# Performance work log

Hardware: AMD Instinct MI355X
Metric: run time of the kernel (lower is better)

The kernel has to match this reference:

```python
import jax, jax.numpy as jnp
import numpy as np

N_NODES = 100000
N_EDGES = 3200000
IN_DIM = 128
H_GCN = 64
H_LSTM = 64


def setup_inputs() -> dict:
    key = jax.random.key(0)
    ks = jax.random.split(key, 12)
    s = 0.05
    return {
        "x": jax.random.normal(ks[0], (IN_DIM, N_NODES), dtype=jnp.float32),
        "edge_index": jax.random.randint(ks[1], (2, N_EDGES), 0, N_NODES, dtype=jnp.int32),
        "W1": jax.random.normal(ks[2], (IN_DIM, H_GCN), dtype=jnp.float32) * s,
        "b1": jnp.zeros((H_GCN,), dtype=jnp.float32),
        "W2": jax.random.normal(ks[3], (H_GCN, H_GCN), dtype=jnp.float32) * s,
        "b2": jnp.zeros((H_GCN,), dtype=jnp.float32),
        "w_ih": jax.random.normal(ks[4], (4 * H_LSTM, H_GCN), dtype=jnp.float32) * s,
        "w_hh": jax.random.normal(ks[5], (4 * H_LSTM, H_LSTM), dtype=jnp.float32) * s,
        "b_ih": jax.random.normal(ks[6], (4 * H_LSTM,), dtype=jnp.float32) * s,
        "b_hh": jax.random.normal(ks[7], (4 * H_LSTM,), dtype=jnp.float32) * s,
        "fc_w": jax.random.normal(ks[8], (1, H_LSTM), dtype=jnp.float32) * s,
        "fc_b": jnp.zeros((1,), dtype=jnp.float32),
    }


def gcn_conv(x, src, dst, n, W, b):
    # PyG GCNConv: add self loops, symmetric norm D^-1/2 (A+I) D^-1/2, linear-first.
    h = x @ W  # [N, out]
    loop = jnp.arange(n, dtype=src.dtype)
    s = jnp.concatenate([src, loop])
    d = jnp.concatenate([dst, loop])
    deg = jax.ops.segment_sum(jnp.ones(d.shape, dtype=h.dtype), d, num_segments=n)
    dinv = jnp.where(deg > 0, jax.lax.rsqrt(deg), 0.0)
    norm = dinv[s] * dinv[d]  # [E+N]
    out = jax.ops.segment_sum(h[s] * norm[:, None], d, num_segments=n)
    return out + b


def reference(x, edge_index, W1, b1, W2, b2, w_ih, w_hh, b_ih, b_hh, fc_w, fc_b):
    xt = x.T  # data.x.T -> [N, input_dim]
    n = xt.shape[0]
    src, dst = edge_index[0], edge_index[1]
    h = jax.nn.relu(gcn_conv(xt, src, dst, n, W1, b1))
    h = gcn_conv(h, src, dst, n, W2, b2)
    z = h[0][None, :]  # [1, H_GCN] node 0 embedding
    # single-step LSTM, zero initial state (h0=c0=0)
    gates = z @ w_ih.T + b_ih + b_hh  # [1, 4H]
    i, f, g, o = jnp.split(gates, 4, axis=-1)
    c = jax.nn.sigmoid(i) * jnp.tanh(g)  # f*c0 = 0
    hy = jax.nn.sigmoid(o) * jnp.tanh(c)  # [1, H_LSTM]
    y = hy @ fc_w.T + fc_b  # [1, 1]
    return y[:, :, None]  # [1, 1, 1]
```

## Files before the change

### kernel.cpp

```cpp
#include <hip/hip_runtime.h>
#include <math.h>

#define N_NODES 100000
#define N_EDGES 3200000
#define IN_DIM 128
#define HG 64

#define E0CAP 2048
#define MCAP  65536
#define NBMW  3125
#define SCAN_BLOCKS 1024
#define BLK_E0 16

#define OFF_DEG       0u
#define OFF_SLOTMAP   400000u
#define OFF_CNT       800000u
#define OFF_ACC       800032u
#define OFF_BMS1      1324320u
#define OFF_BMNEED    1336864u
#define WS_ZERO_BYTES 1349408u
#define OFF_BCNT      1349408u
#define OFF_BLIST     1353504u
#define OFF_EDGES0    1419040u
#define OFF_SLOTNODE  1427232u
#define OFF_MLISTS    1435424u
#define OFF_MLISTD    1697568u

__device__ __forceinline__ float dinv_of(int degv) {
    return 1.0f / sqrtf((float)(degv + 1));
}

__global__ void k_scan0(const int* __restrict__ src, const int* __restrict__ dst,
                        int4* __restrict__ zbase, int* __restrict__ bcnt,
                        int* __restrict__ blist) {
    __shared__ int lcnt;
    __shared__ int lsrc[BLK_E0];
    if (threadIdx.x == 0) lcnt = 0;
    __syncthreads();
    int tid = blockIdx.x * blockDim.x + threadIdx.x;
    int nth = gridDim.x * blockDim.x;
    const int nz = WS_ZERO_BYTES / 16;
    int4 z; z.x = 0; z.y = 0; z.z = 0; z.w = 0;
    for (int i = tid; i < nz; i += nth) zbase[i] = z;
    const int4* dst4 = (const int4*)dst;
    const int n4 = N_EDGES / 4;
    for (int i = tid; i < n4; i += nth) {
        int4 dv = dst4[i];
        int ds[4] = {dv.x, dv.y, dv.z, dv.w};
#pragma unroll
        for (int k = 0; k < 4; k++) {
            if (ds[k] == 0) {
                int p = atomicAdd(&lcnt, 1);
                if (p < BLK_E0) lsrc[p] = src[4 * i + k];
            }
        }
    }
    __syncthreads();
    int c = lcnt; if (c > BLK_E0) c = BLK_E0;
    if (threadIdx.x == 0) bcnt[blockIdx.x] = c;
    for (int i = threadIdx.x; i < c; i += blockDim.x)
        blist[blockIdx.x * BLK_E0 + i] = lsrc[i];
}

__global__ void k_build_slots(const int* __restrict__ bcnt, const int* __restrict__ blist,
                              int* __restrict__ edges0, int* __restrict__ slotnodes,
                              int* __restrict__ slotmap, int* __restrict__ cnt,
                              unsigned* __restrict__ bmS1) {
    const int t = threadIdx.x;
    for (int b = t; b < SCAN_BLOCKS; b += blockDim.x) {
        int c = bcnt[b];
        if (c > 0) {
            int p = atomicAdd(&cnt[0], c);
            for (int j = 0; j < c && p + j < E0CAP; j++)
                edges0[p + j] = blist[b * BLK_E0 + j];
        }
    }
    __syncthreads();
    int n0 = atomicAdd(&cnt[0], 0); if (n0 > E0CAP) n0 = E0CAP;
    for (int i = t; i < n0 + 1; i += blockDim.x) {
        int s = (i == n0) ? 0 : edges0[i];
        if (atomicCAS(&slotmap[s], 0, 1) == 0) {
            int p = atomicAdd(&cnt[1], 1);
            if (p < E0CAP) slotnodes[p] = s;
        }
    }
    __syncthreads();
    int ns = atomicAdd(&cnt[1], 0); if (ns > E0CAP) ns = E0CAP;
    for (int i = t; i < ns; i += blockDim.x) {
        int s = slotnodes[i];
        slotmap[s] = i + 1;
        atomicOr(&bmS1[s >> 5], 1u << (s & 31));
    }
}

__global__ void k_match(const int* __restrict__ src, const int* __restrict__ dst,
                        const int* __restrict__ slotmap,
                        const unsigned* __restrict__ bmS1, unsigned* __restrict__ bmNeed,
                        int* __restrict__ cnt, int* __restrict__ mlistS,
                        int* __restrict__ mlistD) {
    __shared__ unsigned sbm[NBMW];
    for (int i = threadIdx.x; i < NBMW; i += blockDim.x) sbm[i] = bmS1[i];
    __syncthreads();
    int tid = blockIdx.x * blockDim.x + threadIdx.x;
    int nth = gridDim.x * blockDim.x;
    const int4* dst4 = (const int4*)dst;
    const int n4 = N_EDGES / 4;
    for (int i = tid; i < n4; i += nth) {
        int4 dv = dst4[i];
        unsigned ds[4] = {(unsigned)dv.x, (unsigned)dv.y, (unsigned)dv.z, (unsigned)dv.w};
#pragma unroll
        for (int k = 0; k < 4; k++) {
            unsigned d = ds[k];
            if ((sbm[d >> 5] >> (d & 31)) & 1u) {
                int e = 4 * i + k;
                int s = src[e];
                int sl = slotmap[d] - 1;
                int p = atomicAdd(&cnt[2], 1);
                if (p < MCAP) {
                    mlistS[p] = s | (sl << 17);
                    mlistD[p] = (int)d;
                }
                atomicOr(&bmNeed[s >> 5], 1u << (s & 31));
            }
        }
    }
}

__global__ void k_deg_need(const int* __restrict__ dst, const unsigned* __restrict__ bmS1,
                           const unsigned* __restrict__ bmNeed, int* __restrict__ deg) {
    __shared__ unsigned sbm[NBMW];
    for (int i = threadIdx.x; i < NBMW; i += blockDim.x) sbm[i] = bmS1[i] | bmNeed[i];
    __syncthreads();
    int tid = blockIdx.x * blockDim.x + threadIdx.x;
    int nth = gridDim.x * blockDim.x;
    const int4* dst4 = (const int4*)dst;
    const int n4 = N_EDGES / 4;
    for (int i = tid; i < n4; i += nth) {
        int4 dv = dst4[i];
        unsigned ds[4] = {(unsigned)dv.x, (unsigned)dv.y, (unsigned)dv.z, (unsigned)dv.w};
#pragma unroll
        for (int k = 0; k < 4; k++) {
            unsigned d = ds[k];
            if ((sbm[d >> 5] >> (d & 31)) & 1u) atomicAdd(&deg[d], 1);
        }
    }
}

__global__ void k_contrib(const int* __restrict__ deg, const int* __restrict__ cnt,
                          const int* __restrict__ mlistS, const int* __restrict__ mlistD,
                          const int* __restrict__ slotnodes,
                          const float* __restrict__ x, const float* __restrict__ W1,
                          float* __restrict__ acc) {
    int m = cnt[2]; if (m > MCAP) m = MCAP;
    int ns = cnt[1]; if (ns > E0CAP) ns = E0CAP;
    const int vtotal = 2 * (m + ns);
    const int j = threadIdx.x;
    for (int v = blockIdx.x; v < vtotal; v += gridDim.x) {
        const int ii = v >> 1;
        const int kbase = (v & 1) << 6;
        int s, sl;
        float w;
        if (ii < m) {
            int sw = mlistS[ii];
            int d = mlistD[ii];
            s = sw & 0x1FFFF;
            sl = sw >> 17;
            w = dinv_of(deg[s]) * dinv_of(deg[d]);
        } else {
            sl = ii - m;
            s = slotnodes[sl];
            float dv = dinv_of(deg[s]);
            w = dv * dv;
        }
        const float* xp = x + (size_t)kbase * N_NODES + s;
        const float* wp = W1 + kbase * HG + j;
        float g = 0.f;
#pragma unroll
        for (int k = 0; k < 64; k++) {
            g = fmaf(xp[(size_t)k * N_NODES], wp[k * HG], g);
        }
        atomicAdd(&acc[sl * HG + j], g * w);
    }
}

#define CHUNK 256
__global__ void k_final(const float* __restrict__ b1, const float* __restrict__ W2,
                        const float* __restrict__ b2, const float* __restrict__ w_ih,
                        const float* __restrict__ b_ih, const float* __restrict__ b_hh,
                        const float* __restrict__ fc_w, const float* __restrict__ fc_b,
                        const int* __restrict__ deg, const int* __restrict__ slotmap,
                        const int* __restrict__ cnt, const int* __restrict__ edges0,
                        const float* __restrict__ acc, float* __restrict__ out) {
    __shared__ int   sh_sl[CHUNK];
    __shared__ float sh_w[CHUNK];
    __shared__ float partial[4][HG];
    __shared__ float agg[HG];
    __shared__ float zv[HG];
    __shared__ float gates[4 * HG];
    __shared__ float hw[HG];
    const int t = threadIdx.x;
    const int ch = t & (HG - 1);
    const int grp = t >> 6;
    int n0 = cnt[0]; if (n0 > E0CAP) n0 = E0CAP;

    const float dinv0 = dinv_of(deg[0]);
    const float bch = b1[ch];

    float a = 0.f;
    for (int base = 0; base < n0; base += CHUNK) {
        int cn = n0 - base; if (cn > CHUNK) cn = CHUNK;
        __syncthreads();
        if (t < cn) {
            int s = edges0[base + t];
            sh_sl[t] = slotmap[s] - 1;
            sh_w[t] = dinv_of(deg[s]) * dinv0;
        }
        __syncthreads();
        for (int i = grp; i < cn; i += 4) {
            float h = acc[sh_sl[i] * HG + ch] + bch;
            a = fmaf(sh_w[i], (h > 0.f ? h : 0.f), a);
        }
    }
    partial[grp][ch] = a;
    __syncthreads();
    if (t < HG) {
        int sl0 = slotmap[0] - 1;
        float h0 = acc[sl0 * HG + t] + b1[t];
        float s = dinv0 * dinv0 * (h0 > 0.f ? h0 : 0.f);
        s += partial[0][t] + partial[1][t] + partial[2][t] + partial[3][t];
        agg[t] = s;
    }
    __syncthreads();

    if (t < HG) {
        float zz = b2[t];
#pragma unroll 8
        for (int k = 0; k < HG; k++) zz = fmaf(agg[k], W2[k * HG + t], zz);
        zv[t] = zz;
    }
    __syncthreads();

    {
        float gt = b_ih[t] + b_hh[t];
#pragma unroll 8
        for (int jj = 0; jj < HG; jj++) gt = fmaf(zv[jj], w_ih[t * HG + jj], gt);
        gates[t] = gt;
    }
    __syncthreads();

    if (t < HG) {
        float ig = 1.f / (1.f + expf(-gates[t]));
        float gg = tanhf(gates[2 * HG + t]);
        float og = 1.f / (1.f + expf(-gates[3 * HG + t]));
        float c = ig * gg;
        float hy = og * tanhf(c);
        hw[t] = hy * fc_w[t];
    }
    __syncthreads();
    if (t == 0) {
        float y = fc_b[0];
        for (int jj = 0; jj < HG; jj++) y += hw[jj];
        out[0] = y;
    }
}

extern "C" void kernel_launch(void* const* d_in, const int* in_sizes, int n_in,
                              void* d_out, int out_size, void* d_ws, size_t ws_size,
                              hipStream_t stream) {
    const float* x    = (const float*)d_in[0];
    const int*   ei   = (const int*)d_in[1];
    const float* W1   = (const float*)d_in[2];
    const float* b1   = (const float*)d_in[3];
    const float* W2   = (const float*)d_in[4];
    const float* b2   = (const float*)d_in[5];
    const float* w_ih = (const float*)d_in[6];
    const float* b_ih = (const float*)d_in[8];
    const float* b_hh = (const float*)d_in[9];
    const float* fc_w = (const float*)d_in[10];
    const float* fc_b = (const float*)d_in[11];
    float* out = (float*)d_out;

    const int* src = ei;
    const int* dst = ei + N_EDGES;

    char* ws = (char*)d_ws;
    int*      deg       = (int*)(ws + OFF_DEG);
    int*      slotmap   = (int*)(ws + OFF_SLOTMAP);
    int*      cnt       = (int*)(ws + OFF_CNT);
    float*    acc       = (float*)(ws + OFF_ACC);
    unsigned* bmS1      = (unsigned*)(ws + OFF_BMS1);
    unsigned* bmNeed    = (unsigned*)(ws + OFF_BMNEED);
    int*      bcnt      = (int*)(ws + OFF_BCNT);
    int*      blist     = (int*)(ws + OFF_BLIST);
    int*      edges0    = (int*)(ws + OFF_EDGES0);
    int*      slotnodes = (int*)(ws + OFF_SLOTNODE);
    int*      mlistS    = (int*)(ws + OFF_MLISTS);
    int*      mlistD    = (int*)(ws + OFF_MLISTD);

    k_scan0<<<SCAN_BLOCKS, 256, 0, stream>>>(src, dst, (int4*)ws, bcnt, blist);
    k_build_slots<<<1, 256, 0, stream>>>(bcnt, blist, edges0, slotnodes, slotmap, cnt, bmS1);
    k_match<<<SCAN_BLOCKS, 256, 0, stream>>>(src, dst, slotmap, bmS1, bmNeed, cnt,
                                             mlistS, mlistD);
    k_deg_need<<<SCAN_BLOCKS, 256, 0, stream>>>(dst, bmS1, bmNeed, deg);
    k_contrib<<<4096, 64, 0, stream>>>(deg, cnt, mlistS, mlistD, slotnodes, x, W1, acc);
    k_final<<<1, 256, 0, stream>>>(b1, W2, b2, w_ih, b_ih, b_hh, fc_w, fc_b,
                                   deg, slotmap, cnt, edges0, acc, out);
}
```

Baseline: 168.8 us.

## Fuse six-kernel pipeline into one cooperative kernel with grid syncs

Merges the scan, slot-building, match, degree, contribution and final LSTM kernels into a single cooperative launch of 768 blocks that separates phases with grid.sync(). The aim is to remove the launch overhead and inter-kernel gaps of six small launches. Workspace values written by other blocks are now read with atomic reads to keep them coherent across the grid. The cost is grid-wide barriers, fewer blocks for the streaming edge scans, and a contribution phase re-partitioned into four 64-thread workers per block.

```diff
diff --git a/kernel.cpp b/kernel.cpp
--- a/kernel.cpp
+++ b/kernel.cpp
@@ -1,5 +1,8 @@
 #include <hip/hip_runtime.h>
+#include <hip/hip_cooperative_groups.h>
 #include <math.h>
+
+namespace cg = cooperative_groups;
 
 #define N_NODES 100000
 #define N_EDGES 3200000
@@ -9,8 +12,9 @@
 #define E0CAP 2048
 #define MCAP  65536
 #define NBMW  3125
-#define SCAN_BLOCKS 1024
+#define FUSED_BLOCKS 768
 #define BLK_E0 16
+#define CHUNK 256
 
 #define OFF_DEG       0u
 #define OFF_SLOTMAP   400000u
@@ -26,85 +30,98 @@
 #define OFF_MLISTS    1435424u
 #define OFF_MLISTD    1697568u
 
+struct KParams {
+    const int *src, *dst;
+    const float *x, *W1, *b1, *W2, *b2, *w_ih, *b_ih, *b_hh, *fc_w, *fc_b;
+    int *deg, *slotmap, *cnt;
+    float *acc;
+    unsigned *bmS1, *bmNeed;
+    int *bcnt, *blist, *edges0, *slotnodes, *mlistS, *mlistD;
+    float *out;
+};
+
 __device__ __forceinline__ float dinv_of(int degv) {
     return 1.0f / sqrtf((float)(degv + 1));
 }
 
-__global__ void k_scan0(const int* __restrict__ src, const int* __restrict__ dst,
-                        int4* __restrict__ zbase, int* __restrict__ bcnt,
-                        int* __restrict__ blist) {
+__global__ void __launch_bounds__(256, 3) k_fused(KParams p) {
+    cg::grid_group grid = cg::this_grid();
+    __shared__ unsigned sbm[NBMW];
     __shared__ int lcnt;
     __shared__ int lsrc[BLK_E0];
-    if (threadIdx.x == 0) lcnt = 0;
-    __syncthreads();
-    int tid = blockIdx.x * blockDim.x + threadIdx.x;
-    int nth = gridDim.x * blockDim.x;
-    const int nz = WS_ZERO_BYTES / 16;
-    int4 z; z.x = 0; z.y = 0; z.z = 0; z.w = 0;
-    for (int i = tid; i < nz; i += nth) zbase[i] = z;
-    const int4* dst4 = (const int4*)dst;
+    __shared__ int s_m, s_ns;
+    __shared__ int   sh_sl[CHUNK];
+    __shared__ float sh_w[CHUNK];
+    __shared__ float partial[4][HG];
+    __shared__ float agg[HG];
+    __shared__ float zv[HG];
+    __shared__ float gates[4 * HG];
+    __shared__ float hw[HG];
+
+    const int t   = threadIdx.x;
+    const int tid = blockIdx.x * blockDim.x + t;
+    const int nth = gridDim.x * blockDim.x;
+    const int4* dst4 = (const int4*)p.dst;
     const int n4 = N_EDGES / 4;
+
+    if (t == 0) lcnt = 0;
+    __syncthreads();
+    {
+        int4 z; z.x = 0; z.y = 0; z.z = 0; z.w = 0;
+        int4* zb = (int4*)p.deg;
+        const int nz = WS_ZERO_BYTES / 16;
+        for (int i = tid; i < nz; i += nth) zb[i] = z;
+    }
     for (int i = tid; i < n4; i += nth) {
         int4 dv = dst4[i];
         int ds[4] = {dv.x, dv.y, dv.z, dv.w};
 #pragma unroll
         for (int k = 0; k < 4; k++) {
             if (ds[k] == 0) {
-                int p = atomicAdd(&lcnt, 1);
-                if (p < BLK_E0) lsrc[p] = src[4 * i + k];
-            }
-        }
-    }
-    __syncthreads();
-    int c = lcnt; if (c > BLK_E0) c = BLK_E0;
-    if (threadIdx.x == 0) bcnt[blockIdx.x] = c;
-    for (int i = threadIdx.x; i < c; i += blockDim.x)
-        blist[blockIdx.x * BLK_E0 + i] = lsrc[i];
-}
-
-__global__ void k_build_slots(const int* __restrict__ bcnt, const int* __restrict__ blist,
-                              int* __restrict__ edges0, int* __restrict__ slotnodes,
-                              int* __restrict__ slotmap, int* __restrict__ cnt,
-                              unsigned* __restrict__ bmS1) {
-    const int t = threadIdx.x;
-    for (int b = t; b < SCAN_BLOCKS; b += blockDim.x) {
-        int c = bcnt[b];
-        if (c > 0) {
-            int p = atomicAdd(&cnt[0], c);
-            for (int j = 0; j < c && p + j < E0CAP; j++)
-                edges0[p + j] = blist[b * BLK_E0 + j];
-        }
-    }
-    __syncthreads();
-    int n0 = atomicAdd(&cnt[0], 0); if (n0 > E0CAP) n0 = E0CAP;
-    for (int i = t; i < n0 + 1; i += blockDim.x) {
-        int s = (i == n0) ? 0 : edges0[i];
-        if (atomicCAS(&slotmap[s], 0, 1) == 0) {
-            int p = atomicAdd(&cnt[1], 1);
-            if (p < E0CAP) slotnodes[p] = s;
-        }
-    }
-    __syncthreads();
-    int ns = atomicAdd(&cnt[1], 0); if (ns > E0CAP) ns = E0CAP;
-    for (int i = t; i < ns; i += blockDim.x) {
-        int s = slotnodes[i];
-        slotmap[s] = i + 1;
-        atomicOr(&bmS1[s >> 5], 1u << (s & 31));
-    }
-}
-
-__global__ void k_match(const int* __restrict__ src, const int* __restrict__ dst,
-                        const int* __restrict__ slotmap,
-                        const unsigned* __restrict__ bmS1, unsigned* __restrict__ bmNeed,
-                        int* __restrict__ cnt, int* __restrict__ mlistS,
-                        int* __restrict__ mlistD) {
-    __shared__ unsigned sbm[NBMW];
-    for (int i = threadIdx.x; i < NBMW; i += blockDim.x) sbm[i] = bmS1[i];
-    __syncthreads();
-    int tid = blockIdx.x * blockDim.x + threadIdx.x;
-    int nth = gridDim.x * blockDim.x;
-    const int4* dst4 = (const int4*)dst;
-    const int n4 = N_EDGES / 4;
+                int q = atomicAdd(&lcnt, 1);
+                if (q < BLK_E0) lsrc[q] = p.src[4 * i + k];
+            }
+        }
+    }
+    __syncthreads();
+    {
+        int c = lcnt; if (c > BLK_E0) c = BLK_E0;
+        if (t == 0) p.bcnt[blockIdx.x] = c;
+        for (int i = t; i < c; i += blockDim.x)
+            p.blist[blockIdx.x * BLK_E0 + i] = lsrc[i];
+    }
+    grid.sync();
+
+    if (blockIdx.x == 0) {
+        for (int b = t; b < FUSED_BLOCKS; b += blockDim.x) {
+            int c = p.bcnt[b];
+            if (c > 0) {
+                int q = atomicAdd(&p.cnt[0], c);
+                for (int j = 0; j < c && q + j < E0CAP; j++)
+                    p.edges0[q + j] = p.blist[b * BLK_E0 + j];
+            }
+        }
+        __syncthreads();
+        int n0 = atomicAdd(&p.cnt[0], 0); if (n0 > E0CAP) n0 = E0CAP;
+        for (int i = t; i < n0 + 1; i += blockDim.x) {
+            int s = (i == n0) ? 0 : p.edges0[i];
+            if (atomicCAS(&p.slotmap[s], 0, 1) == 0) {
+                int q = atomicAdd(&p.cnt[1], 1);
+                if (q < E0CAP) p.slotnodes[q] = s;
+            }
+        }
+        __syncthreads();
+        int ns = atomicAdd(&p.cnt[1], 0); if (ns > E0CAP) ns = E0CAP;
+        for (int i = t; i < ns; i += blockDim.x) {
+            int s = p.slotnodes[i];
+            p.slotmap[s] = i + 1;
+            atomicOr(&p.bmS1[s >> 5], 1u << (s & 31));
+        }
+    }
+    grid.sync();
+
+    for (int i = t; i < NBMW; i += blockDim.x) sbm[i] = p.bmS1[i];
+    __syncthreads();
     for (int i = tid; i < n4; i += nth) {
         int4 dv = dst4[i];
         unsigned ds[4] = {(unsigned)dv.x, (unsigned)dv.y, (unsigned)dv.z, (unsigned)dv.w};
@@ -113,196 +130,172 @@
             unsigned d = ds[k];
             if ((sbm[d >> 5] >> (d & 31)) & 1u) {
                 int e = 4 * i + k;
-                int s = src[e];
-                int sl = slotmap[d] - 1;
-                int p = atomicAdd(&cnt[2], 1);
-                if (p < MCAP) {
-                    mlistS[p] = s | (sl << 17);
-                    mlistD[p] = (int)d;
+                int s = p.src[e];
+                int sl = atomicAdd(&p.slotmap[d], 0) - 1;
+                int q = atomicAdd(&p.cnt[2], 1);
+                if (q < MCAP) {
+                    p.mlistS[q] = s | (sl << 17);
+                    p.mlistD[q] = (int)d;
                 }
-                atomicOr(&bmNeed[s >> 5], 1u << (s & 31));
-            }
-        }
-    }
-}
-
-__global__ void k_deg_need(const int* __restrict__ dst, const unsigned* __restrict__ bmS1,
-                           const unsigned* __restrict__ bmNeed, int* __restrict__ deg) {
-    __shared__ unsigned sbm[NBMW];
-    for (int i = threadIdx.x; i < NBMW; i += blockDim.x) sbm[i] = bmS1[i] | bmNeed[i];
-    __syncthreads();
-    int tid = blockIdx.x * blockDim.x + threadIdx.x;
-    int nth = gridDim.x * blockDim.x;
-    const int4* dst4 = (const int4*)dst;
-    const int n4 = N_EDGES / 4;
+                atomicOr(&p.bmNeed[s >> 5], 1u << (s & 31));
+            }
+        }
+    }
+    grid.sync();
+
+    for (int i = t; i < NBMW; i += blockDim.x) sbm[i] = p.bmS1[i] | p.bmNeed[i];
+    __syncthreads();
     for (int i = tid; i < n4; i += nth) {
         int4 dv = dst4[i];
         unsigned ds[4] = {(unsigned)dv.x, (unsigned)dv.y, (unsigned)dv.z, (unsigned)dv.w};
 #pragma unroll
         for (int k = 0; k < 4; k++) {
             unsigned d = ds[k];
-            if ((sbm[d >> 5] >> (d & 31)) & 1u) atomicAdd(&deg[d], 1);
-        }
-    }
-}
-
-__global__ void k_contrib(const int* __restrict__ deg, const int* __restrict__ cnt,
-                          const int* __restrict__ mlistS, const int* __restrict__ mlistD,
-                          const int* __restrict__ slotnodes,
-                          const float* __restrict__ x, const float* __restrict__ W1,
-                          float* __restrict__ acc) {
-    int m = cnt[2]; if (m > MCAP) m = MCAP;
-    int ns = cnt[1]; if (ns > E0CAP) ns = E0CAP;
-    const int vtotal = 2 * (m + ns);
-    const int j = threadIdx.x;
-    for (int v = blockIdx.x; v < vtotal; v += gridDim.x) {
-        const int ii = v >> 1;
-        const int kbase = (v & 1) << 6;
-        int s, sl;
-        float w;
-        if (ii < m) {
-            int sw = mlistS[ii];
-            int d = mlistD[ii];
-            s = sw & 0x1FFFF;
-            sl = sw >> 17;
-            w = dinv_of(deg[s]) * dinv_of(deg[d]);
-        } else {
-            sl = ii - m;
-            s = slotnodes[sl];
-            float dv = dinv_of(deg[s]);
-            w = dv * dv;
-        }
-        const float* xp = x + (size_t)kbase * N_NODES + s;
-        const float* wp = W1 + kbase * HG + j;
-        float g = 0.f;
+            if ((sbm[d >> 5] >> (d & 31)) & 1u) atomicAdd(&p.deg[d], 1);
+        }
+    }
+    grid.sync();
+
+    if (t == 0) {
+        int m = atomicAdd(&p.cnt[2], 0); if (m > MCAP) m = MCAP;
+        int ns = atomicAdd(&p.cnt[1], 0); if (ns > E0CAP) ns = E0CAP;
+        s_m = m; s_ns = ns;
+    }
+    __syncthreads();
+    {
+        const int m = s_m, ns = s_ns;
+        const int vtotal = 2 * (m + ns);
+        const int j = t & 63;
+        const int wk = (blockIdx.x << 2) | (t >> 6);
+        const int nwk = gridDim.x << 2;
+        for (int v = wk; v < vtotal; v += nwk) {
+            const int ii = v >> 1;
+            const int kbase = (v & 1) << 6;
+            int s, sl;
+            float w;
+            if (ii < m) {
+                int sw = p.mlistS[ii];
+                int d = p.mlistD[ii];
+                s = sw & 0x1FFFF;
+                sl = sw >> 17;
+                w = dinv_of(atomicAdd(&p.deg[s], 0)) * dinv_of(atomicAdd(&p.deg[d], 0));
+            } else {
+                sl = ii - m;
+                s = p.slotnodes[sl];
+                float dv = dinv_of(atomicAdd(&p.deg[s], 0));
+                w = dv * dv;
+            }
+            const float* xp = p.x + (size_t)kbase * N_NODES + s;
+            const float* wp = p.W1 + kbase * HG + j;
+            float g = 0.f;
 #pragma unroll
-        for (int k = 0; k < 64; k++) {
-            g = fmaf(xp[(size_t)k * N_NODES], wp[k * HG], g);
-        }
-        atomicAdd(&acc[sl * HG + j], g * w);
-    }
-}
-
-#define CHUNK 256
-__global__ void k_final(const float* __restrict__ b1, const float* __restrict__ W2,
-                        const float* __restrict__ b2, const float* __restrict__ w_ih,
-                        const float* __restrict__ b_ih, const float* __restrict__ b_hh,
-                        const float* __restrict__ fc_w, const float* __restrict__ fc_b,
-                        const int* __restrict__ deg, const int* __restrict__ slotmap,
-                        const int* __restrict__ cnt, const int* __restrict__ edges0,
-                        const float* __restrict__ acc, float* __restrict__ out) {
-    __shared__ int   sh_sl[CHUNK];
-    __shared__ float sh_w[CHUNK];
-    __shared__ float partial[4][HG];
-    __shared__ float agg[HG];
-    __shared__ float zv[HG];
-    __shared__ float gates[4 * HG];
-    __shared__ float hw[HG];
-    const int t = threadIdx.x;
-    const int ch = t & (HG - 1);
-    const int grp = t >> 6;
-    int n0 = cnt[0]; if (n0 > E0CAP) n0 = E0CAP;
-
-    const float dinv0 = dinv_of(deg[0]);
-    const float bch = b1[ch];
-
-    float a = 0.f;
-    for (int base = 0; base < n0; base += CHUNK) {
-        int cn = n0 - base; if (cn > CHUNK) cn = CHUNK;
-        __syncthreads();
-        if (t < cn) {
-            int s = edges0[base + t];
-            sh_sl[t] = slotmap[s] - 1;
-            sh_w[t] = dinv_of(deg[s]) * dinv0;
-        }
-        __syncthreads();
-        for (int i = grp; i < cn; i += 4) {
-            float h = acc[sh_sl[i] * HG + ch] + bch;
-            a = fmaf(sh_w[i], (h > 0.f ? h : 0.f), a);
-        }
-    }
-    partial[grp][ch] = a;
-    __syncthreads();
-    if (t < HG) {
-        int sl0 = slotmap[0] - 1;
-        float h0 = acc[sl0 * HG + t] + b1[t];
-        float s = dinv0 * dinv0 * (h0 > 0.f ? h0 : 0.f);
-        s += partial[0][t] + partial[1][t] + partial[2][t] + partial[3][t];
-        agg[t] = s;
-    }
-    __syncthreads();
-
-    if (t < HG) {
-        float zz = b2[t];
+            for (int k = 0; k < 64; k++) {
+                g = fmaf(xp[(size_t)k * N_NODES], wp[k * HG], g);
+            }
+            atomicAdd(&p.acc[sl * HG + j], g * w);
+        }
+    }
+    grid.sync();
+
+    if (blockIdx.x != 0) return;
+    {
+        const int ch = t & (HG - 1);
+        const int grp = t >> 6;
+        int n0 = p.cnt[0]; if (n0 > E0CAP) n0 = E0CAP;
+        const float dinv0 = dinv_of(atomicAdd(&p.deg[0], 0));
+        const float bch = p.b1[ch];
+
+        float a = 0.f;
+        for (int base = 0; base < n0; base += CHUNK) {
+            int cn = n0 - base; if (cn > CHUNK) cn = CHUNK;
+            __syncthreads();
+            if (t < cn) {
+                int s = p.edges0[base + t];
+                sh_sl[t] = atomicAdd(&p.slotmap[s], 0) - 1;
+                sh_w[t] = dinv_of(atomicAdd(&p.deg[s], 0)) * dinv0;
+            }
+            __syncthreads();
+            for (int i = grp; i < cn; i += 4) {
+                float h = atomicAdd(&p.acc[sh_sl[i] * HG + ch], 0.f) + bch;
+                a = fmaf(sh_w[i], (h > 0.f ? h : 0.f), a);
+            }
+        }
+        partial[grp][ch] = a;
+        __syncthreads();
+        if (t < HG) {
+            int sl0 = atomicAdd(&p.slotmap[0], 0) - 1;
+            float h0 = atomicAdd(&p.acc[sl0 * HG + t], 0.f) + p.b1[t];
+            float s = dinv0 * dinv0 * (h0 > 0.f ? h0 : 0.f);
+            s += partial[0][t] + partial[1][t] + partial[2][t] + partial[3][t];
+            agg[t] = s;
+        }
+        __syncthreads();
+
+        if (t < HG) {
+            float zz = p.b2[t];
 #pragma unroll 8
-        for (int k = 0; k < HG; k++) zz = fmaf(agg[k], W2[k * HG + t], zz);
-        zv[t] = zz;
-    }
-    __syncthreads();
-
-    {
-        float gt = b_ih[t] + b_hh[t];
+            for (int k = 0; k < HG; k++) zz = fmaf(agg[k], p.W2[k * HG + t], zz);
+            zv[t] = zz;
+        }
+        __syncthreads();
+
+        {
+            float gt = p.b_ih[t] + p.b_hh[t];
 #pragma unroll 8
-        for (int jj = 0; jj < HG; jj++) gt = fmaf(zv[jj], w_ih[t * HG + jj], gt);
-        gates[t] = gt;
-    }
-    __syncthreads();
-
-    if (t < HG) {
-        float ig = 1.f / (1.f + expf(-gates[t]));
-        float gg = tanhf(gates[2 * HG + t]);
-        float og = 1.f / (1.f + expf(-gates[3 * HG + t]));
-        float c = ig * gg;
-        float hy = og * tanhf(c);
-        hw[t] = hy * fc_w[t];
-    }
-    __syncthreads();
-    if (t == 0) {
-        float y = fc_b[0];
-        for (int jj = 0; jj < HG; jj++) y += hw[jj];
-        out[0] = y;
+            for (int jj = 0; jj < HG; jj++) gt = fmaf(zv[jj], p.w_ih[t * HG + jj], gt);
+            gates[t] = gt;
+        }
+        __syncthreads();
+
+        if (t < HG) {
+            float ig = 1.f / (1.f + expf(-gates[t]));
+            float gg = tanhf(gates[2 * HG + t]);
+            float og = 1.f / (1.f + expf(-gates[3 * HG + t]));
+            float c = ig * gg;
+            float hy = og * tanhf(c);
+            hw[t] = hy * p.fc_w[t];
+        }
+        __syncthreads();
+        if (t == 0) {
+            float y = p.fc_b[0];
+            for (int jj = 0; jj < HG; jj++) y += hw[jj];
+            p.out[0] = y;
+        }
     }
 }
 
 extern "C" void kernel_launch(void* const* d_in, const int* in_sizes, int n_in,
                               void* d_out, int out_size, void* d_ws, size_t ws_size,
                               hipStream_t stream) {
-    const float* x    = (const float*)d_in[0];
-    const int*   ei   = (const int*)d_in[1];
-    const float* W1   = (const float*)d_in[2];
-    const float* b1   = (const float*)d_in[3];
-    const float* W2   = (const float*)d_in[4];
-    const float* b2   = (const float*)d_in[5];
-    const float* w_ih = (const float*)d_in[6];
-    const float* b_ih = (const float*)d_in[8];
-    const float* b_hh = (const float*)d_in[9];
-    const float* fc_w = (const float*)d_in[10];
-    const float* fc_b = (const float*)d_in[11];
-    float* out = (float*)d_out;
-
-    const int* src = ei;
-    const int* dst = ei + N_EDGES;
-
     char* ws = (char*)d_ws;
-    int*      deg       = (int*)(ws + OFF_DEG);
-    int*      slotmap   = (int*)(ws + OFF_SLOTMAP);
-    int*      cnt       = (int*)(ws + OFF_CNT);
-    float*    acc       = (float*)(ws + OFF_ACC);
-    unsigned* bmS1      = (unsigned*)(ws + OFF_BMS1);
-    unsigned* bmNeed    = (unsigned*)(ws + OFF_BMNEED);
-    int*      bcnt      = (int*)(ws + OFF_BCNT);
-    int*      blist     = (int*)(ws + OFF_BLIST);
-    int*      edges0    = (int*)(ws + OFF_EDGES0);
-    int*      slotnodes = (int*)(ws + OFF_SLOTNODE);
-    int*      mlistS    = (int*)(ws + OFF_MLISTS);
-    int*      mlistD    = (int*)(ws + OFF_MLISTD);
-
-    k_scan0<<<SCAN_BLOCKS, 256, 0, stream>>>(src, dst, (int4*)ws, bcnt, blist);
-    k_build_slots<<<1, 256, 0, stream>>>(bcnt, blist, edges0, slotnodes, slotmap, cnt, bmS1);
-    k_match<<<SCAN_BLOCKS, 256, 0, stream>>>(src, dst, slotmap, bmS1, bmNeed, cnt,
-                                             mlistS, mlistD);
-    k_deg_need<<<SCAN_BLOCKS, 256, 0, stream>>>(dst, bmS1, bmNeed, deg);
-    k_contrib<<<4096, 64, 0, stream>>>(deg, cnt, mlistS, mlistD, slotnodes, x, W1, acc);
-    k_final<<<1, 256, 0, stream>>>(b1, W2, b2, w_ih, b_ih, b_hh, fc_w, fc_b,
-                                   deg, slotmap, cnt, edges0, acc, out);
+    KParams P;
+    P.src   = (const int*)d_in[1];
+    P.dst   = ((const int*)d_in[1]) + N_EDGES;
+    P.x     = (const float*)d_in[0];
+    P.W1    = (const float*)d_in[2];
+    P.b1    = (const float*)d_in[3];
+    P.W2    = (const float*)d_in[4];
+    P.b2    = (const float*)d_in[5];
+    P.w_ih  = (const float*)d_in[6];
+    P.b_ih  = (const float*)d_in[8];
+    P.b_hh  = (const float*)d_in[9];
+    P.fc_w  = (const float*)d_in[10];
+    P.fc_b  = (const float*)d_in[11];
+    P.deg       = (int*)(ws + OFF_DEG);
+    P.slotmap   = (int*)(ws + OFF_SLOTMAP);
+    P.cnt       = (int*)(ws + OFF_CNT);
+    P.acc       = (float*)(ws + OFF_ACC);
+    P.bmS1      = (unsigned*)(ws + OFF_BMS1);
+    P.bmNeed    = (unsigned*)(ws + OFF_BMNEED);
+    P.bcnt      = (int*)(ws + OFF_BCNT);
+    P.blist     = (int*)(ws + OFF_BLIST);
+    P.edges0    = (int*)(ws + OFF_EDGES0);
+    P.slotnodes = (int*)(ws + OFF_SLOTNODE);
+    P.mlistS    = (int*)(ws + OFF_MLISTS);
+    P.mlistD    = (int*)(ws + OFF_MLISTD);
+    P.out   = (float*)d_out;
+
+    void* kargs[] = { (void*)&P };
+    hipLaunchCooperativeKernel((void*)k_fused, dim3(FUSED_BLOCKS), dim3(256),
+                               kargs, 0, stream);
 }
```

Result: slower. 581.8 us (+244.7%).

## Fuse degree counting with x@W1 contributions; defer normalization to final kernel

Applied to the files above, without the earlier changes.

Merges the degree-count and x@W1 contribution kernels into one launch split by block index, so the gather-heavy matvec work runs at the same time as the degree atomics. The contributions no longer depend on degrees: raw per-edge partial products are written to a gbuf buffer, and the single-block final kernel applies normalization, scatters into shared-memory slot windows and aggregates. This removes one launch and the global atomic accumulation. In exchange, the serial single-block final kernel now rescans the whole match list once per 64-slot window, and gbuf costs extra memory traffic.

```diff
diff --git a/kernel.cpp b/kernel.cpp
--- a/kernel.cpp
+++ b/kernel.cpp
@@ -11,20 +11,21 @@
 #define NBMW  3125
 #define SCAN_BLOCKS 1024
 #define BLK_E0 16
+#define DC_BLOCKS 2048
 
 #define OFF_DEG       0u
 #define OFF_SLOTMAP   400000u
 #define OFF_CNT       800000u
-#define OFF_ACC       800032u
-#define OFF_BMS1      1324320u
-#define OFF_BMNEED    1336864u
-#define WS_ZERO_BYTES 1349408u
-#define OFF_BCNT      1349408u
-#define OFF_BLIST     1353504u
-#define OFF_EDGES0    1419040u
-#define OFF_SLOTNODE  1427232u
-#define OFF_MLISTS    1435424u
-#define OFF_MLISTD    1697568u
+#define OFF_BMS1      800032u
+#define OFF_BMNEED    812576u
+#define WS_ZERO_BYTES 825120u
+#define OFF_BCNT      825120u
+#define OFF_BLIST     829216u
+#define OFF_EDGES0    894752u
+#define OFF_SLOTNODE  902944u
+#define OFF_MLISTS    911136u
+#define OFF_MLISTD    1173280u
+#define OFF_GBUF      1435424u
 
 __device__ __forceinline__ float dinv_of(int degv) {
     return 1.0f / sqrtf((float)(degv + 1));
@@ -126,116 +127,130 @@
     }
 }
 
-__global__ void k_deg_need(const int* __restrict__ dst, const unsigned* __restrict__ bmS1,
-                           const unsigned* __restrict__ bmNeed, int* __restrict__ deg) {
-    __shared__ unsigned sbm[NBMW];
-    for (int i = threadIdx.x; i < NBMW; i += blockDim.x) sbm[i] = bmS1[i] | bmNeed[i];
-    __syncthreads();
-    int tid = blockIdx.x * blockDim.x + threadIdx.x;
-    int nth = gridDim.x * blockDim.x;
-    const int4* dst4 = (const int4*)dst;
-    const int n4 = N_EDGES / 4;
-    for (int i = tid; i < n4; i += nth) {
-        int4 dv = dst4[i];
-        unsigned ds[4] = {(unsigned)dv.x, (unsigned)dv.y, (unsigned)dv.z, (unsigned)dv.w};
+__global__ void k_deg_contrib(const int* __restrict__ dst,
+                              const unsigned* __restrict__ bmS1,
+                              const unsigned* __restrict__ bmNeed,
+                              int* __restrict__ deg,
+                              const int* __restrict__ cnt,
+                              const int* __restrict__ mlistS,
+                              const int* __restrict__ slotnodes,
+                              const float* __restrict__ x, const float* __restrict__ W1,
+                              float* __restrict__ gbuf) {
+    if (blockIdx.x < 1024) {
+        __shared__ unsigned sbm[NBMW];
+        for (int i = threadIdx.x; i < NBMW; i += blockDim.x) sbm[i] = bmS1[i] | bmNeed[i];
+        __syncthreads();
+        int tid = blockIdx.x * blockDim.x + threadIdx.x;
+        int nth = 1024 * blockDim.x;
+        const int4* dst4 = (const int4*)dst;
+        const int n4 = N_EDGES / 4;
+        for (int i = tid; i < n4; i += nth) {
+            int4 dv = dst4[i];
+            unsigned ds[4] = {(unsigned)dv.x, (unsigned)dv.y, (unsigned)dv.z, (unsigned)dv.w};
 #pragma unroll
-        for (int k = 0; k < 4; k++) {
-            unsigned d = ds[k];
-            if ((sbm[d >> 5] >> (d & 31)) & 1u) atomicAdd(&deg[d], 1);
-        }
-    }
-}
-
-__global__ void k_contrib(const int* __restrict__ deg, const int* __restrict__ cnt,
-                          const int* __restrict__ mlistS, const int* __restrict__ mlistD,
-                          const int* __restrict__ slotnodes,
-                          const float* __restrict__ x, const float* __restrict__ W1,
-                          float* __restrict__ acc) {
-    int m = cnt[2]; if (m > MCAP) m = MCAP;
-    int ns = cnt[1]; if (ns > E0CAP) ns = E0CAP;
-    const int vtotal = 2 * (m + ns);
-    const int j = threadIdx.x;
-    for (int v = blockIdx.x; v < vtotal; v += gridDim.x) {
-        const int ii = v >> 1;
-        const int kbase = (v & 1) << 6;
-        int s, sl;
-        float w;
-        if (ii < m) {
-            int sw = mlistS[ii];
-            int d = mlistD[ii];
-            s = sw & 0x1FFFF;
-            sl = sw >> 17;
-            w = dinv_of(deg[s]) * dinv_of(deg[d]);
-        } else {
-            sl = ii - m;
-            s = slotnodes[sl];
-            float dv = dinv_of(deg[s]);
-            w = dv * dv;
-        }
-        const float* xp = x + (size_t)kbase * N_NODES + s;
-        const float* wp = W1 + kbase * HG + j;
-        float g = 0.f;
+            for (int k = 0; k < 4; k++) {
+                unsigned d = ds[k];
+                if ((sbm[d >> 5] >> (d & 31)) & 1u) atomicAdd(&deg[d], 1);
+            }
+        }
+    } else {
+        int m = cnt[2]; if (m > MCAP) m = MCAP;
+        int ns = cnt[1]; if (ns > E0CAP) ns = E0CAP;
+        const int vtotal = 2 * (m + ns);
+        const int j = threadIdx.x & 63;
+        const int bk = blockIdx.x - 1024;
+        const int wk = (bk << 2) | (threadIdx.x >> 6);
+        const int nwk = 1024 << 2;
+        for (int v = wk; v < vtotal; v += nwk) {
+            const int ii = v >> 1;
+            const int kbase = (v & 1) << 6;
+            int s;
+            if (ii < m) s = mlistS[ii] & 0x1FFFF;
+            else        s = slotnodes[ii - m];
+            const float* xp = x + (size_t)kbase * N_NODES + s;
+            const float* wp = W1 + kbase * HG + j;
+            float g = 0.f;
 #pragma unroll
-        for (int k = 0; k < 64; k++) {
-            g = fmaf(xp[(size_t)k * N_NODES], wp[k * HG], g);
-        }
-        atomicAdd(&acc[sl * HG + j], g * w);
-    }
-}
-
-#define CHUNK 256
+            for (int k = 0; k < 64; k++) {
+                g = fmaf(xp[(size_t)k * N_NODES], wp[k * HG], g);
+            }
+            gbuf[(size_t)v * HG + j] = g;
+        }
+    }
+}
+
+#define SLOTW 64
 __global__ void k_final(const float* __restrict__ b1, const float* __restrict__ W2,
                         const float* __restrict__ b2, const float* __restrict__ w_ih,
                         const float* __restrict__ b_ih, const float* __restrict__ b_hh,
                         const float* __restrict__ fc_w, const float* __restrict__ fc_b,
                         const int* __restrict__ deg, const int* __restrict__ slotmap,
                         const int* __restrict__ cnt, const int* __restrict__ edges0,
-                        const float* __restrict__ acc, float* __restrict__ out) {
-    __shared__ int   sh_sl[CHUNK];
-    __shared__ float sh_w[CHUNK];
-    __shared__ float partial[4][HG];
-    __shared__ float agg[HG];
+                        const int* __restrict__ mlistS, const int* __restrict__ mlistD,
+                        const int* __restrict__ slotnodes,
+                        const float* __restrict__ gbuf, float* __restrict__ out) {
+    __shared__ float hacc[SLOTW][HG];
+    __shared__ float aggs[HG];
     __shared__ float zv[HG];
     __shared__ float gates[4 * HG];
     __shared__ float hw[HG];
     const int t = threadIdx.x;
-    const int ch = t & (HG - 1);
-    const int grp = t >> 6;
+    const int j = t & 63;
+    const int wv = t >> 6;
+
+    int m  = cnt[2]; if (m > MCAP) m = MCAP;
+    int ns = cnt[1]; if (ns > E0CAP) ns = E0CAP;
     int n0 = cnt[0]; if (n0 > E0CAP) n0 = E0CAP;
-
+    const int total = m + ns;
     const float dinv0 = dinv_of(deg[0]);
-    const float bch = b1[ch];
-
-    float a = 0.f;
-    for (int base = 0; base < n0; base += CHUNK) {
-        int cn = n0 - base; if (cn > CHUNK) cn = CHUNK;
+    const int sl0 = slotmap[0] - 1;
+    const float bj = b1[j];
+
+    if (t < HG) aggs[t] = 0.f;
+
+    for (int wb = 0; wb < ns; wb += SLOTW) {
         __syncthreads();
-        if (t < cn) {
-            int s = edges0[base + t];
-            sh_sl[t] = slotmap[s] - 1;
-            sh_w[t] = dinv_of(deg[s]) * dinv0;
-        }
+        for (int i = t; i < SLOTW * HG; i += 256) ((float*)hacc)[i] = 0.f;
         __syncthreads();
-        for (int i = grp; i < cn; i += 4) {
-            float h = acc[sh_sl[i] * HG + ch] + bch;
-            a = fmaf(sh_w[i], (h > 0.f ? h : 0.f), a);
-        }
-    }
-    partial[grp][ch] = a;
-    __syncthreads();
-    if (t < HG) {
-        int sl0 = slotmap[0] - 1;
-        float h0 = acc[sl0 * HG + t] + b1[t];
-        float s = dinv0 * dinv0 * (h0 > 0.f ? h0 : 0.f);
-        s += partial[0][t] + partial[1][t] + partial[2][t] + partial[3][t];
-        agg[t] = s;
+        for (int ii = wv; ii < total; ii += 4) {
+            int s, sl;
+            float w;
+            if (ii < m) {
+                int sw = mlistS[ii];
+                s = sw & 0x1FFFF;
+                sl = sw >> 17;
+                if (sl < wb || sl >= wb + SLOTW) continue;
+                w = dinv_of(deg[s]) * dinv_of(deg[mlistD[ii]]);
+            } else {
+                sl = ii - m;
+                if (sl < wb || sl >= wb + SLOTW) continue;
+                s = slotnodes[sl];
+                float dv = dinv_of(deg[s]);
+                w = dv * dv;
+            }
+            float g = gbuf[(size_t)(2 * ii) * HG + j] + gbuf[(size_t)(2 * ii + 1) * HG + j];
+            atomicAdd(&hacc[sl - wb][j], g * w);
+        }
+        __syncthreads();
+        for (int i = wv; i < n0; i += 4) {
+            int s = edges0[i];
+            int sl = slotmap[s] - 1;
+            if (sl < wb || sl >= wb + SLOTW) continue;
+            float w2 = dinv_of(deg[s]) * dinv0;
+            float h = hacc[sl - wb][j] + bj;
+            atomicAdd(&aggs[j], w2 * (h > 0.f ? h : 0.f));
+        }
+        if (wv == 0 && sl0 >= wb && sl0 < wb + SLOTW) {
+            float h0 = hacc[sl0 - wb][j] + bj;
+            atomicAdd(&aggs[j], dinv0 * dinv0 * (h0 > 0.f ? h0 : 0.f));
+        }
     }
     __syncthreads();
 
     if (t < HG) {
         float zz = b2[t];
 #pragma unroll 8
-        for (int k = 0; k < HG; k++) zz = fmaf(agg[k], W2[k * HG + t], zz);
+        for (int k = 0; k < HG; k++) zz = fmaf(aggs[k], W2[k * HG + t], zz);
         zv[t] = zz;
     }
     __syncthreads();
@@ -287,7 +302,6 @@
     int*      deg       = (int*)(ws + OFF_DEG);
     int*      slotmap   = (int*)(ws + OFF_SLOTMAP);
     int*      cnt       = (int*)(ws + OFF_CNT);
-    float*    acc       = (float*)(ws + OFF_ACC);
     unsigned* bmS1      = (unsigned*)(ws + OFF_BMS1);
     unsigned* bmNeed    = (unsigned*)(ws + OFF_BMNEED);
     int*      bcnt      = (int*)(ws + OFF_BCNT);
@@ -296,13 +310,15 @@
     int*      slotnodes = (int*)(ws + OFF_SLOTNODE);
     int*      mlistS    = (int*)(ws + OFF_MLISTS);
     int*      mlistD    = (int*)(ws + OFF_MLISTD);
+    float*    gbuf      = (float*)(ws + OFF_GBUF);
 
     k_scan0<<<SCAN_BLOCKS, 256, 0, stream>>>(src, dst, (int4*)ws, bcnt, blist);
     k_build_slots<<<1, 256, 0, stream>>>(bcnt, blist, edges0, slotnodes, slotmap, cnt, bmS1);
     k_match<<<SCAN_BLOCKS, 256, 0, stream>>>(src, dst, slotmap, bmS1, bmNeed, cnt,
                                              mlistS, mlistD);
-    k_deg_need<<<SCAN_BLOCKS, 256, 0, stream>>>(dst, bmS1, bmNeed, deg);
-    k_contrib<<<4096, 64, 0, stream>>>(deg, cnt, mlistS, mlistD, slotnodes, x, W1, acc);
+    k_deg_contrib<<<DC_BLOCKS, 256, 0, stream>>>(dst, bmS1, bmNeed, deg, cnt, mlistS,
+                                                 slotnodes, x, W1, gbuf);
     k_final<<<1, 256, 0, stream>>>(b1, W2, b2, w_ih, b_ih, b_hh, fc_w, fc_b,
-                                   deg, slotmap, cnt, edges0, acc, out);
-}
+                                   deg, slotmap, cnt, edges0, mlistS, mlistD,
+                                   slotnodes, gbuf, out);
+}
```

Result: slower. 425.3 us (+152.0%).
